# Optimization experiments

Hardware: AMD Instinct MI355X
Metric: run time of the kernel (lower is better)

The kernel has to match this reference:

```python
import jax, jax.numpy as jnp
import numpy as np

INPUT_DIM = 1024
OUT_DIM = 128


def setup_inputs() -> dict:
    key = jax.random.key(0)
    ks = jax.random.split(key, 9)
    B, N, M, d, din = 8, 256, 256, OUT_DIM, INPUT_DIM
    s = lambda fan_in: 1.0 / np.sqrt(fan_in)
    return {
        "X": jax.random.normal(ks[0], (B, N, d), dtype=jnp.float32),
        "Y": jax.random.normal(ks[1], (B, M, d), dtype=jnp.float32),
        "weights": jax.random.normal(ks[2], (B, din), dtype=jnp.float32),
        # nn.Linear(input_dim, output_dim) -> A_w [d, din], A_b [d]
        "A_w": jax.random.uniform(ks[3], (d, din), jnp.float32, -s(din), s(din)),
        "A_b": jax.random.uniform(ks[4], (d,), jnp.float32, -s(din), s(din)),
        # nn.Linear(2d, d)
        "lin_w": jax.random.uniform(ks[5], (d, 2 * d), jnp.float32, -s(2 * d), s(2 * d)),
        "lin_b": jax.random.uniform(ks[6], (d,), jnp.float32, -s(2 * d), s(2 * d)),
        # nn.Linear(d, 1)
        "out_w": jax.random.uniform(ks[7], (1, d), jnp.float32, -s(d), s(d)),
        "out_b": jax.random.uniform(ks[8], (1,), jnp.float32, -s(d), s(d)),
    }


def reference(X, Y, weights, A_w, A_b, lin_w, lin_b, out_w, out_b):
    # forward_complex path (dropout in eval mode = identity).
    # coefficients: [B, 1, d]
    coeff = jnp.tanh(weights @ A_w.T + A_b)[:, None, :]
    Xc = X * coeff  # [B, N, d]
    # complex_lin applied to cat([Xc_repeated, Y_repeated], -1) decomposes as
    # a sum of two low-rank projections broadcast over the pairwise grid,
    # avoiding the [B, N, M, 2d] concat tensor.
    Wx = lin_w[:, :X.shape[-1]]   # [d, d]
    Wy = lin_w[:, X.shape[-1]:]   # [d, d]
    px = jnp.einsum('bnd,ed->bne', Xc, Wx)  # [B, N, d]
    py = jnp.einsum('bmd,ed->bme', Y, Wy)   # [B, M, d]
    U1 = px[:, :, None, :] + py[:, None, :, :] + lin_b  # [B, N, M, d]
    U2 = jax.nn.relu(U1)
    out = jnp.einsum('bnmd,od->bnmo', U2, out_w) + out_b  # [B, N, M, 1]
    return out[..., 0]
```

## Files before the change

### kernel.cpp

```cpp
#include <hip/hip_runtime.h>


#define B_ 8
#define NM 256
#define D_ 128
#define DIN 1024

typedef _Float16 hh;
typedef _Float16 hh2 __attribute__((ext_vector_type(2)));
struct __attribute__((aligned(16))) H8 { hh2 h[4]; };

__device__ __forceinline__ float dot2acc(hh2 a, hh2 b, float c) {
#if __has_builtin(__builtin_amdgcn_fdot2)
    return __builtin_amdgcn_fdot2(a, b, c, false);
#else
    return c + (float)a.x * (float)b.x + (float)a.y * (float)b.y;
#endif
}

__global__ void k_coeff(const float* __restrict__ W, const float* __restrict__ Aw,
                        const float* __restrict__ Ab, float* __restrict__ coeff) {
    int wid  = (blockIdx.x * blockDim.x + threadIdx.x) >> 6;
    int lane = threadIdx.x & 63;
    int b = wid >> 7, e = wid & 127;
    const float4* wr = (const float4*)(W + b * DIN);
    const float4* ar = (const float4*)(Aw + (size_t)e * DIN);
    float s = 0.f;
#pragma unroll
    for (int i = 0; i < 4; ++i) {
        float4 wv = wr[i * 64 + lane];
        float4 av = ar[i * 64 + lane];
        s += wv.x * av.x + wv.y * av.y + wv.z * av.z + wv.w * av.w;
    }
#pragma unroll
    for (int d = 32; d; d >>= 1) s += __shfl_xor(s, d, 64);
    if (lane == 0) coeff[b * 128 + e] = tanhf(s + Ab[e]);
}

__global__ __launch_bounds__(512) void k_proj(
    const float* __restrict__ X, const float* __restrict__ Y,
    const float* __restrict__ coeff, const float* __restrict__ lin_w,
    const float* __restrict__ lin_b, const float* __restrict__ out_w,
    hh* __restrict__ px, hh* __restrict__ pyc,
    float* __restrict__ qx, float* __restrict__ qy)
{
    __shared__ __align__(16) char smem[66816];
    float* S   = (float*)smem;
    float* Wl  = (float*)(smem + 8448);
    float* RED = (float*)(smem + 42240);

    const int bx = blockIdx.x;
    const int bsrc = bx >> 4, b = bsrc >> 1, src = bsrc & 1;
    const int r0 = (bx & 15) * 16;
    const int t = threadIdx.x;

    const float* Sg = (src ? Y : X) + (size_t)(b * NM + r0) * D_;
    {
        float4 v = ((const float4*)Sg)[t];
        if (!src) {
            float4 c = ((const float4*)(coeff + b * 128))[t & 31];
            v.x *= c.x; v.y *= c.y; v.z *= c.z; v.w *= c.w;
        }
        *(float4*)(&S[(t >> 5) * 132 + (t & 31) * 4]) = v;
    }

    const int kq = t >> 7, tt = t & 127;
    const int er = tt & 31, rr = tt >> 5;
    float acc[4][4] = {};

    for (int p = 0; p < 2; ++p) {
        __syncthreads();
        for (int ii = t; ii < 2048; ii += 512) {
            int e = ii >> 4, k4 = ii & 15;
            float4 g = *(const float4*)(lin_w + (size_t)e * 256 + src * 128 +
                                        p * 64 + k4 * 4);
            float* wp = &Wl[e * 66 + k4 * 4];
            *(float2*)(wp)     = make_float2(g.x, g.y);
            *(float2*)(wp + 2) = make_float2(g.z, g.w);
        }
        __syncthreads();
#pragma unroll
        for (int kt = 0; kt < 16; kt += 4) {
            const int kl = kq * 16 + kt;
            const int kg = p * 64 + kl;
            float4 a[4]; float2 w0[4], w1[4];
#pragma unroll
            for (int i = 0; i < 4; ++i)
                a[i] = *(const float4*)(&S[(rr + 4 * i) * 132 + kg]);
#pragma unroll
            for (int j = 0; j < 4; ++j) {
                const float* wp = &Wl[(er + 32 * j) * 66 + kl];
                w0[j] = *(const float2*)(wp);
                w1[j] = *(const float2*)(wp + 2);
            }
#pragma unroll
            for (int i = 0; i < 4; ++i)
#pragma unroll
                for (int j = 0; j < 4; ++j)
                    acc[i][j] += a[i].x * w0[j].x + a[i].y * w0[j].y +
                                 a[i].z * w1[j].x + a[i].w * w1[j].y;
        }
    }

    __syncthreads();
    if (kq) {
        float* R = RED + (size_t)(kq - 1) * 2048;
#pragma unroll
        for (int i = 0; i < 4; ++i)
#pragma unroll
            for (int j = 0; j < 4; ++j) R[(i * 4 + j) * 128 + tt] = acc[i][j];
    }
    __syncthreads();
    if (kq == 0) {
#pragma unroll
        for (int q = 0; q < 3; ++q)
#pragma unroll
            for (int i = 0; i < 4; ++i)
#pragma unroll
                for (int j = 0; j < 4; ++j)
                    acc[i][j] += RED[(size_t)q * 2048 + (i * 4 + j) * 128 + tt];
        hh* Pg = (src ? pyc : px) + (size_t)(b * NM + r0) * D_;
        float qpart[4] = {0.f, 0.f, 0.f, 0.f};
#pragma unroll
        for (int i = 0; i < 4; ++i)
#pragma unroll
            for (int j = 0; j < 4; ++j) {
                int e = er + 32 * j;
                float v = acc[i][j];
                if (src) v += lin_b[e];
                Pg[(rr + 4 * i) * D_ + e] = (hh)v;
                qpart[i] = fmaf(0.5f * out_w[e], v, qpart[i]);
            }
        float* Qg = (src ? qy : qx) + b * NM + r0;
#pragma unroll
        for (int i = 0; i < 4; ++i) {
            float s = qpart[i];
#pragma unroll
            for (int d2 = 16; d2; d2 >>= 1) s += __shfl_xor(s, d2, 64);
            if (er == 0) Qg[rr + 4 * i] = s;
        }
    }
}

__global__ __launch_bounds__(512) void k_main(
    const hh* __restrict__ px, const hh* __restrict__ pyc,
    const float* __restrict__ qx, const float* __restrict__ qy,
    const float* __restrict__ out_w, const float* __restrict__ out_b,
    float* __restrict__ out) {
    __shared__ hh PXs[64 * 136];
    __shared__ hh PYs[32 * 136];
    __shared__ float RED[48 * 128];
    __shared__ hh WHs[128];
    __shared__ float QXl[64], QYl[32];

    const int bx = blockIdx.x;
    const int b = bx & 7, tile = bx >> 3;
    const int n0 = (tile >> 3) * 64, m0 = (tile & 7) * 32;
    const int t = threadIdx.x;

    const uint4* pxg = (const uint4*)(px + (size_t)(b * NM + n0) * D_);
    for (int i = t; i < 1024; i += 512)
        *(uint4*)(&PXs[(i >> 4) * 136 + (i & 15) * 8]) = pxg[i];
    const uint4* pyg = (const uint4*)(pyc + (size_t)(b * NM + m0) * D_);
    if (t < 512)
        *(uint4*)(&PYs[(t >> 4) * 136 + (t & 15) * 8]) = pyg[t];
    if (t < 128) WHs[t] = (hh)(0.5f * out_w[t]);
    else if (t < 192) QXl[t - 128] = qx[b * NM + n0 + (t - 128)];
    else if (t < 224) QYl[t - 192] = qy[b * NM + m0 + (t - 192)];
    __syncthreads();

    const int w = t >> 6, eq = w & 3, half = w >> 2;
    const int s = half * 64 + (t & 63);
    const int nr = s >> 3, mr = s & 7;
    const int e0 = eq * 32;

    hh2 wv[16];
#pragma unroll
    for (int q = 0; q < 16; ++q) wv[q] = *(const hh2*)(&WHs[e0 + 2 * q]);

    float acc[4][4] = {};
#pragma unroll
    for (int es = 0; es < 4; ++es) {
        H8 xa[4], ya[4];
#pragma unroll
        for (int i = 0; i < 4; ++i)
            xa[i] = *(const H8*)(&PXs[(nr + 16 * i) * 136 + e0 + es * 8]);
#pragma unroll
        for (int j = 0; j < 4; ++j)
            ya[j] = *(const H8*)(&PYs[(mr + 8 * j) * 136 + e0 + es * 8]);
#pragma unroll
        for (int i = 0; i < 4; ++i)
#pragma unroll
            for (int j = 0; j < 4; ++j)
#pragma unroll
                for (int p = 0; p < 4; ++p) {
                    hh2 u = xa[i].h[p] + ya[j].h[p];
                    unsigned uu;
                    __builtin_memcpy(&uu, &u, 4);
                    uu &= 0x7fff7fffu;
                    hh2 au;
                    __builtin_memcpy(&au, &uu, 4);
                    acc[i][j] = dot2acc(au, wv[es * 4 + p], acc[i][j]);
                }
    }

    if (eq) {
#pragma unroll
        for (int i = 0; i < 4; ++i)
#pragma unroll
            for (int j = 0; j < 4; ++j)
                RED[((eq - 1) * 16 + i * 4 + j) * 128 + s] = acc[i][j];
    }
    __syncthreads();
    if (eq == 0) {
        const float ob = out_b[0];
        float* og = out + (size_t)b * NM * NM;
#pragma unroll
        for (int i = 0; i < 4; ++i) {
            float qn = QXl[nr + 16 * i];
#pragma unroll
            for (int j = 0; j < 4; ++j) {
                float v = acc[i][j];
#pragma unroll
                for (int p = 0; p < 3; ++p)
                    v += RED[(p * 16 + i * 4 + j) * 128 + s];
                og[(n0 + nr + 16 * i) * NM + m0 + mr + 8 * j] =
                    v + qn + QYl[mr + 8 * j] + ob;
            }
        }
    }
}

extern "C" void kernel_launch(void* const* d_in, const int* in_sizes, int n_in,
                              void* d_out, int out_size, void* d_ws, size_t ws_size,
                              hipStream_t stream) {
    const float* X      = (const float*)d_in[0];
    const float* Y      = (const float*)d_in[1];
    const float* wts    = (const float*)d_in[2];
    const float* A_w    = (const float*)d_in[3];
    const float* A_b    = (const float*)d_in[4];
    const float* lin_w  = (const float*)d_in[5];
    const float* lin_b  = (const float*)d_in[6];
    const float* out_w  = (const float*)d_in[7];
    const float* out_b  = (const float*)d_in[8];
    float* out = (float*)d_out;

    hh*    px    = (hh*)d_ws;
    hh*    pyc   = px + B_ * NM * D_;
    float* qx    = (float*)(pyc + B_ * NM * D_);
    float* qy    = qx + 2048;
    float* coeff = qy + 2048;

    k_coeff<<<256, 256, 0, stream>>>(wts, A_w, A_b, coeff);
    k_proj<<<dim3(256), 512, 0, stream>>>(X, Y, coeff, lin_w, lin_b, out_w,
                                          px, pyc, qx, qy);
    k_main<<<dim3(256), 512, 0, stream>>>(px, pyc, qx, qy, out_w, out_b, out);
}
```

Before: 24.39 us.

## Merge coeff computation with Y projection and use fp16 dot2 projections

```diff
diff --git a/kernel.cpp b/kernel.cpp
--- a/kernel.cpp
+++ b/kernel.cpp
@@ -8,6 +8,7 @@
 
 typedef _Float16 hh;
 typedef _Float16 hh2 __attribute__((ext_vector_type(2)));
+struct __attribute__((aligned(8)))  H4 { hh2 h[2]; };
 struct __attribute__((aligned(16))) H8 { hh2 h[4]; };
 
 __device__ __forceinline__ float dot2acc(hh2 a, hh2 b, float c) {
@@ -18,88 +19,87 @@
 #endif
 }
 
-__global__ void k_coeff(const float* __restrict__ W, const float* __restrict__ Aw,
-                        const float* __restrict__ Ab, float* __restrict__ coeff) {
-    int wid  = (blockIdx.x * blockDim.x + threadIdx.x) >> 6;
-    int lane = threadIdx.x & 63;
-    int b = wid >> 7, e = wid & 127;
-    const float4* wr = (const float4*)(W + b * DIN);
-    const float4* ar = (const float4*)(Aw + (size_t)e * DIN);
-    float s = 0.f;
-#pragma unroll
-    for (int i = 0; i < 4; ++i) {
-        float4 wv = wr[i * 64 + lane];
-        float4 av = ar[i * 64 + lane];
-        s += wv.x * av.x + wv.y * av.y + wv.z * av.z + wv.w * av.w;
-    }
-#pragma unroll
-    for (int d = 32; d; d >>= 1) s += __shfl_xor(s, d, 64);
-    if (lane == 0) coeff[b * 128 + e] = tanhf(s + Ab[e]);
-}
-
-__global__ __launch_bounds__(512) void k_proj(
-    const float* __restrict__ X, const float* __restrict__ Y,
-    const float* __restrict__ coeff, const float* __restrict__ lin_w,
-    const float* __restrict__ lin_b, const float* __restrict__ out_w,
-    hh* __restrict__ px, hh* __restrict__ pyc,
-    float* __restrict__ qx, float* __restrict__ qy)
+__device__ __forceinline__ void st_h4(hh* p, float4 v) {
+    H4 h;
+    h.h[0] = hh2{(hh)v.x, (hh)v.y};
+    h.h[1] = hh2{(hh)v.z, (hh)v.w};
+    *(H4*)p = h;
+}
+
+__global__ __launch_bounds__(512) void k1(
+    const float* __restrict__ Y, const float* __restrict__ wts,
+    const float* __restrict__ Aw, const float* __restrict__ Ab,
+    const float* __restrict__ lin_w, const float* __restrict__ lin_b,
+    const float* __restrict__ out_w, float* __restrict__ coeff,
+    hh* __restrict__ pyc, float* __restrict__ qy)
 {
-    __shared__ __align__(16) char smem[66816];
-    float* S   = (float*)smem;
-    float* Wl  = (float*)(smem + 8448);
-    float* RED = (float*)(smem + 42240);
+    __shared__ hh S[16 * 136];
+    __shared__ hh Wl[128 * 132];
+    __shared__ float RED[3 * 2048];
 
     const int bx = blockIdx.x;
-    const int bsrc = bx >> 4, b = bsrc >> 1, src = bsrc & 1;
-    const int r0 = (bx & 15) * 16;
     const int t = threadIdx.x;
 
-    const float* Sg = (src ? Y : X) + (size_t)(b * NM + r0) * D_;
+    if (bx < 128) {
+        const int w = t >> 6, lane = t & 63;
+        const int job = bx * 8 + w;
+        const int b = job >> 7, e = job & 127;
+        const float4* wr = (const float4*)(wts + b * DIN);
+        const float4* ar = (const float4*)(Aw + (size_t)e * DIN);
+        float s = 0.f;
+#pragma unroll
+        for (int i = 0; i < 4; ++i) {
+            float4 wv = wr[i * 64 + lane];
+            float4 av = ar[i * 64 + lane];
+            s += wv.x * av.x + wv.y * av.y + wv.z * av.z + wv.w * av.w;
+        }
+#pragma unroll
+        for (int d = 32; d; d >>= 1) s += __shfl_xor(s, d, 64);
+        if (lane == 0) coeff[b * 128 + e] = tanhf(s + Ab[e]);
+        return;
+    }
+
+    const int bb = bx - 128;
+    const int b = bb >> 4, r0 = (bb & 15) * 16;
+
     {
-        float4 v = ((const float4*)Sg)[t];
-        if (!src) {
-            float4 c = ((const float4*)(coeff + b * 128))[t & 31];
-            v.x *= c.x; v.y *= c.y; v.z *= c.z; v.w *= c.w;
-        }
-        *(float4*)(&S[(t >> 5) * 132 + (t & 31) * 4]) = v;
-    }
+        float4 v = ((const float4*)(Y + (size_t)(b * NM + r0) * D_))[t];
+        st_h4(&S[(t >> 5) * 136 + (t & 31) * 4], v);
+    }
+    for (int ii = t; ii < 4096; ii += 512) {
+        int e = ii >> 5, k4 = ii & 31;
+        float4 g = *(const float4*)(lin_w + (size_t)e * 256 + 128 + k4 * 4);
+        st_h4(&Wl[e * 132 + k4 * 4], g);
+    }
+    __syncthreads();
 
     const int kq = t >> 7, tt = t & 127;
     const int er = tt & 31, rr = tt >> 5;
     float acc[4][4] = {};
-
-    for (int p = 0; p < 2; ++p) {
-        __syncthreads();
-        for (int ii = t; ii < 2048; ii += 512) {
-            int e = ii >> 4, k4 = ii & 15;
-            float4 g = *(const float4*)(lin_w + (size_t)e * 256 + src * 128 +
-                                        p * 64 + k4 * 4);
-            float* wp = &Wl[e * 66 + k4 * 4];
-            *(float2*)(wp)     = make_float2(g.x, g.y);
-            *(float2*)(wp + 2) = make_float2(g.z, g.w);
-        }
-        __syncthreads();
-#pragma unroll
-        for (int kt = 0; kt < 16; kt += 4) {
-            const int kl = kq * 16 + kt;
-            const int kg = p * 64 + kl;
-            float4 a[4]; float2 w0[4], w1[4];
-#pragma unroll
-            for (int i = 0; i < 4; ++i)
-                a[i] = *(const float4*)(&S[(rr + 4 * i) * 132 + kg]);
-#pragma unroll
-            for (int j = 0; j < 4; ++j) {
-                const float* wp = &Wl[(er + 32 * j) * 66 + kl];
-                w0[j] = *(const float2*)(wp);
-                w1[j] = *(const float2*)(wp + 2);
-            }
-#pragma unroll
-            for (int i = 0; i < 4; ++i)
-#pragma unroll
-                for (int j = 0; j < 4; ++j)
-                    acc[i][j] += a[i].x * w0[j].x + a[i].y * w0[j].y +
-                                 a[i].z * w1[j].x + a[i].w * w1[j].y;
-        }
+#pragma unroll
+    for (int kt = 0; kt < 32; kt += 8) {
+        const int kg = kq * 32 + kt;
+        H8 a[4]; H4 w0[4], w1[4];
+#pragma unroll
+        for (int i = 0; i < 4; ++i)
+            a[i] = *(const H8*)(&S[(rr + 4 * i) * 136 + kg]);
+#pragma unroll
+        for (int j = 0; j < 4; ++j) {
+            const hh* wp = &Wl[(er + 32 * j) * 132 + kg];
+            w0[j] = *(const H4*)(wp);
+            w1[j] = *(const H4*)(wp + 4);
+        }
+#pragma unroll
+        for (int i = 0; i < 4; ++i)
+#pragma unroll
+            for (int j = 0; j < 4; ++j) {
+                float c = acc[i][j];
+                c = dot2acc(a[i].h[0], w0[j].h[0], c);
+                c = dot2acc(a[i].h[1], w0[j].h[1], c);
+                c = dot2acc(a[i].h[2], w1[j].h[0], c);
+                c = dot2acc(a[i].h[3], w1[j].h[1], c);
+                acc[i][j] = c;
+            }
     }
 
     __syncthreads();
@@ -119,21 +119,114 @@
 #pragma unroll
                 for (int j = 0; j < 4; ++j)
                     acc[i][j] += RED[(size_t)q * 2048 + (i * 4 + j) * 128 + tt];
-        hh* Pg = (src ? pyc : px) + (size_t)(b * NM + r0) * D_;
+        hh* Pg = pyc + (size_t)(b * NM + r0) * D_;
         float qpart[4] = {0.f, 0.f, 0.f, 0.f};
 #pragma unroll
         for (int i = 0; i < 4; ++i)
+#pragma unroll
+            for (int j = 0; j < 4; ++j) {
+                int e = er + 32 * j;
+                float v = acc[i][j] + lin_b[e];
+                Pg[(rr + 4 * i) * D_ + e] = (hh)v;
+                qpart[i] = fmaf(0.5f * out_w[e], v, qpart[i]);
+            }
+        float* Qg = qy + b * NM + r0;
+#pragma unroll
+        for (int i = 0; i < 4; ++i) {
+            float s = qpart[i];
+#pragma unroll
+            for (int d2 = 16; d2; d2 >>= 1) s += __shfl_xor(s, d2, 64);
+            if (er == 0) Qg[rr + 4 * i] = s;
+        }
+    }
+}
+
+__global__ __launch_bounds__(512) void k2(
+    const float* __restrict__ X, const float* __restrict__ coeff,
+    const float* __restrict__ lin_w, const float* __restrict__ out_w,
+    hh* __restrict__ px, float* __restrict__ qx)
+{
+    __shared__ hh S[8 * 136];
+    __shared__ hh Wl[128 * 132];
+    __shared__ float RED[3 * 1024];
+
+    const int bx = blockIdx.x;
+    const int b = bx >> 5, r0 = (bx & 31) * 8;
+    const int t = threadIdx.x;
+
+    if (t < 256) {
+        float4 v = ((const float4*)(X + (size_t)(b * NM + r0) * D_))[t];
+        float4 c = ((const float4*)(coeff + b * 128))[t & 31];
+        v.x *= c.x; v.y *= c.y; v.z *= c.z; v.w *= c.w;
+        st_h4(&S[(t >> 5) * 136 + (t & 31) * 4], v);
+    }
+    for (int ii = t; ii < 4096; ii += 512) {
+        int e = ii >> 5, k4 = ii & 31;
+        float4 g = *(const float4*)(lin_w + (size_t)e * 256 + k4 * 4);
+        st_h4(&Wl[e * 132 + k4 * 4], g);
+    }
+    __syncthreads();
+
+    const int kq = t >> 7, tt = t & 127;
+    const int er = tt & 31, rr = tt >> 5;
+    float acc[2][4] = {};
+#pragma unroll
+    for (int kt = 0; kt < 32; kt += 8) {
+        const int kg = kq * 32 + kt;
+        H8 a[2]; H4 w0[4], w1[4];
+#pragma unroll
+        for (int i = 0; i < 2; ++i)
+            a[i] = *(const H8*)(&S[(rr + 4 * i) * 136 + kg]);
+#pragma unroll
+        for (int j = 0; j < 4; ++j) {
+            const hh* wp = &Wl[(er + 32 * j) * 132 + kg];
+            w0[j] = *(const H4*)(wp);
+            w1[j] = *(const H4*)(wp + 4);
+        }
+#pragma unroll
+        for (int i = 0; i < 2; ++i)
+#pragma unroll
+            for (int j = 0; j < 4; ++j) {
+                float c = acc[i][j];
+                c = dot2acc(a[i].h[0], w0[j].h[0], c);
+                c = dot2acc(a[i].h[1], w0[j].h[1], c);
+                c = dot2acc(a[i].h[2], w1[j].h[0], c);
+                c = dot2acc(a[i].h[3], w1[j].h[1], c);
+                acc[i][j] = c;
+            }
+    }
+
+    __syncthreads();
+    if (kq) {
+        float* R = RED + (size_t)(kq - 1) * 1024;
+#pragma unroll
+        for (int i = 0; i < 2; ++i)
+#pragma unroll
+            for (int j = 0; j < 4; ++j) R[(i * 4 + j) * 128 + tt] = acc[i][j];
+    }
+    __syncthreads();
+    if (kq == 0) {
+#pragma unroll
+        for (int q = 0; q < 3; ++q)
+#pragma unroll
+            for (int i = 0; i < 2; ++i)
+#pragma unroll
+                for (int j = 0; j < 4; ++j)
+                    acc[i][j] += RED[(size_t)q * 1024 + (i * 4 + j) * 128 + tt];
+        hh* Pg = px + (size_t)(b * NM + r0) * D_;
+        float qpart[2] = {0.f, 0.f};
+#pragma unroll
+        for (int i = 0; i < 2; ++i)
 #pragma unroll
             for (int j = 0; j < 4; ++j) {
                 int e = er + 32 * j;
                 float v = acc[i][j];
-                if (src) v += lin_b[e];
                 Pg[(rr + 4 * i) * D_ + e] = (hh)v;
                 qpart[i] = fmaf(0.5f * out_w[e], v, qpart[i]);
             }
-        float* Qg = (src ? qy : qx) + b * NM + r0;
-#pragma unroll
-        for (int i = 0; i < 4; ++i) {
+        float* Qg = qx + b * NM + r0;
+#pragma unroll
+        for (int i = 0; i < 2; ++i) {
             float s = qpart[i];
 #pragma unroll
             for (int d2 = 16; d2; d2 >>= 1) s += __shfl_xor(s, d2, 64);
@@ -251,8 +344,8 @@
     float* qy    = qx + 2048;
     float* coeff = qy + 2048;
 
-    k_coeff<<<256, 256, 0, stream>>>(wts, A_w, A_b, coeff);
-    k_proj<<<dim3(256), 512, 0, stream>>>(X, Y, coeff, lin_w, lin_b, out_w,
-                                          px, pyc, qx, qy);
+    k1<<<dim3(256), 512, 0, stream>>>(Y, wts, A_w, A_b, lin_w, lin_b, out_w,
+                                      coeff, pyc, qy);
+    k2<<<dim3(256), 512, 0, stream>>>(X, coeff, lin_w, out_w, px, qx);
     k_main<<<dim3(256), 512, 0, stream>>>(px, pyc, qx, qy, out_w, out_b, out);
 }
```

After: 21.02 us. 1.16x faster.
